# Performance work log

Hardware: AMD Instinct MI355X
Metric: run time of the kernel (lower is better)

Reference implementation:

```python
import jax, jax.numpy as jnp
import numpy as np

LEAKY_SLOPE = 0.01  # torch nn.LeakyReLU default

def leaky_relu(x):
    return jnp.where(x >= 0, x, LEAKY_SLOPE * x)

def setup_inputs() -> dict:
    key = jax.random.key(0)
    ks = jax.random.split(key, 11)
    B, F, C_IN, H, K, D = 2048, 512, 3, 64, 8, 128  # batch, features, expand, layer_conf[0], bucket_num, bucket_dim
    ASR, MM, OUT = 128, 768, 256
    proj_in = ASR + MM + F * D
    inp = {
        "stat_features": jax.random.uniform(ks[0], (B, F), dtype=jnp.float32),
        "asr_embeddings": jax.random.normal(ks[1], (B, ASR), dtype=jnp.float32),
        "mm_embeddings": jax.random.normal(ks[2], (B, MM), dtype=jnp.float32),
        "linear1_w": jax.random.normal(ks[3], (F, C_IN, H), dtype=jnp.float32) * (1.0 / np.sqrt(C_IN)),
        "linear1_b": jax.random.normal(ks[4], (F, 1, H), dtype=jnp.float32),
        "linear2_w": jax.random.normal(ks[5], (F, H, K), dtype=jnp.float32) * (1.0 / np.sqrt(H)),
        "linear2_b": jax.random.normal(ks[6], (F, 1, K), dtype=jnp.float32),
        "tau": jnp.ones((F, 1, K), dtype=jnp.float32),
        "emb": jax.random.normal(ks[7], (F, K, D), dtype=jnp.float32),
        "proj_w": jax.random.normal(ks[8], (OUT, proj_in), dtype=jnp.float32) * (1.0 / np.sqrt(proj_in)),
        "proj_b": jax.random.normal(ks[9], (OUT,), dtype=jnp.float32) * 0.01,
    }
    return inp

def reference(stat_features, asr_embeddings, mm_embeddings,
              linear1_w, linear1_b, linear2_w, linear2_b, tau, emb,
              proj_w, proj_b):
    # sanitize: NaN -> 0, negatives -> 0
    x = stat_features
    x = jnp.where(jnp.isnan(x) | (x < 0.0), 0.0, x)  # [B, F]

    # auto_dis: per-feature tiny MLP. x is expanded to 3 identical copies -> [B,F,1,3]
    # matmul with [F,3,H] == einsum over the 3 copies.
    B, F = x.shape
    x3 = jnp.broadcast_to(x[:, :, None], (B, F, 3))           # [B,F,3]
    h = jnp.einsum('bfc,fch->bfh', x3, linear1_w) + linear1_b[:, 0, :]  # [B,F,H]
    h = jnp.where(h >= 0, h, LEAKY_SLOPE * h)
    s = jnp.einsum('bfh,fhk->bfk', h, linear2_w) + linear2_b[:, 0, :]   # [B,F,K]
    s = jnp.where(s >= 0, s, LEAKY_SLOPE * s)
    s = s * tau[:, 0, :]
    p = jax.nn.softmax(s, axis=-1)                            # [B,F,K]
    y = jnp.einsum('bfk,fkd->bfd', p, emb)                    # [B,F,D]
    y = y.reshape(B, -1)                                      # [B, F*D] (fc = Identity)

    z = jnp.concatenate([asr_embeddings, mm_embeddings, y], axis=1)
    out = jax.nn.relu(z @ proj_w.T + proj_b)                  # [B, 256]
    return out
```

## Files before the change

kernel.cpp:

```cpp
#include <hip/hip_runtime.h>
#include <hip/hip_bf16.h>
#include <math.h>

#define LEAKY 0.01f
#define B_    2048
#define F_    512
#define H_    64
#define K_    8
#define D_    128
#define ASR_  128
#define MM_   768
#define OUT_  256
#define PROJ_IN 66432
#define ZK    4992
#define NSPLIT 8


typedef unsigned short u16;
typedef u16   u16x8 __attribute__((ext_vector_type(8)));
typedef short s16x8 __attribute__((ext_vector_type(8)));
typedef float f32x4 __attribute__((ext_vector_type(4)));

__device__ __forceinline__ u16 f2bf(float x) {
  unsigned int u = __float_as_uint(x);
  u += 0x7fffu + ((u >> 16) & 1u);
  return (u16)(u >> 16);
}

#define PRODUCER_BLOCKS (512 + 1024 + 896 + 224)
#define QS 40
#define FS 164

__global__ __launch_bounds__(256) void producer_kernel(
    const float* __restrict__ stat, const float* __restrict__ w1,
    const float* __restrict__ b1v, const float* __restrict__ w2,
    const float* __restrict__ b2v, const float* __restrict__ tauv,
    const float* __restrict__ pw, const float* __restrict__ emb,
    const float* __restrict__ asr, const float* __restrict__ mm,
    u16* __restrict__ A0, u16* __restrict__ Pf, u16* __restrict__ Wn) {
  __shared__ __align__(16) char smem[15616];
  const int bid = blockIdx.x;
  const int t = threadIdx.x;

  if (bid < 512) {
    const int f0 = (bid >> 3) * 8;
    const int o0 = (bid & 7) * 32;
    float* s_pw = (float*)smem;
    const int fl = t >> 5, k = (t >> 2) & 7, dq = t & 3;
    float4 e[8];
    {
      const float* ep = emb + ((size_t)(f0 + fl) * 8 + k) * 128 + dq * 32;
      #pragma unroll
      for (int j = 0; j < 8; ++j) e[j] = *(const float4*)(ep + j * 4);
    }
    const int cq = (t >> 3) & 3, ci = t & 7;
    const int wofs = (t >> 5) * FS + cq * QS + ci * 4;
    const float* pwbase = pw + 896 + (size_t)f0 * 128 + (size_t)o0 * PROJ_IN + t * 4;
#define LD(R) (*(const float4*)(pwbase + (size_t)(R) * PROJ_IN))
    float4 nx0 = LD(0), nx1 = LD(1), nx2 = LD(2);
    *(float4*)(s_pw + wofs) = nx0;
    nx0 = LD(3);
    asm volatile("s_waitcnt lgkmcnt(0)" ::: "memory");
    __builtin_amdgcn_s_barrier();
    u16* wdst = Wn + (size_t)o0 * ZK + 896 + (size_t)(f0 + fl) * 8 + k;
    for (int r = 0; r < 32; ++r) {
      float* buf  = s_pw + (r & 1) * (8 * FS);
      float* nbuf = s_pw + ((r + 1) & 1) * (8 * FS);
      if (r + 1 < 32) *(float4*)(nbuf + wofs) = nx1;
      nx1 = nx2; nx2 = nx0;
      if (r + 4 < 32) nx0 = LD(r + 4);
      const float* pp = buf + fl * FS + dq * QS;
      float gp0 = 0.f, gp1 = 0.f;
      #pragma unroll
      for (int j = 0; j < 8; ++j) {
        float4 p4 = *(const float4*)(pp + j * 4);
        gp0 = fmaf(e[j].x, p4.x, gp0);
        gp1 = fmaf(e[j].y, p4.y, gp1);
        gp0 = fmaf(e[j].z, p4.z, gp0);
        gp1 = fmaf(e[j].w, p4.w, gp1);
      }
      float g = gp0 + gp1;
      g += __shfl_xor(g, 1);
      g += __shfl_xor(g, 2);
      if (dq == 0) wdst[(size_t)r * ZK] = f2bf(g);
      asm volatile("s_waitcnt lgkmcnt(0)" ::: "memory");
      __builtin_amdgcn_s_barrier();
    }
#undef LD
  } else if (bid < 1536) {
    const int pb = bid - 512;
    const int f0 = (pb & 127) * 4;
    const int b0 = (pb >> 7) * 256;
    float* s_w1s = (float*)(smem);
    float* s_b1  = (float*)(smem + 1024);
    float* s_w2  = (float*)(smem + 2048);
    float* s_b2  = (float*)(smem + 10240);
    float* s_tau = (float*)(smem + 10368);
    float* s_x   = (float*)(smem + 10496);
    {
      int fl = t >> 6, h = t & 63;
      const float* wf = w1 + (size_t)(f0 + fl) * 192;
      s_w1s[fl * 64 + h] = wf[h] + wf[64 + h] + wf[128 + h];
      s_b1[fl * 64 + h] = b1v[(size_t)(f0 + fl) * 64 + h];
    }
    for (int i = t; i < 4 * 512; i += 256) {
      int fl = i >> 9, idx = i & 511;
      s_w2[fl * 512 + idx] = w2[(size_t)(f0 + fl) * 512 + idx];
    }
    if (t < 32) {
      s_b2[t]  = b2v[f0 * 8 + t];
      s_tau[t] = tauv[f0 * 8 + t];
    }
    {
      float4 sv = *(const float4*)(stat + (size_t)(b0 + t) * F_ + f0);
      float* xr = s_x + t * 5;
      xr[0] = (sv.x >= 0.f) ? sv.x : 0.f;
      xr[1] = (sv.y >= 0.f) ? sv.y : 0.f;
      xr[2] = (sv.z >= 0.f) ? sv.z : 0.f;
      xr[3] = (sv.w >= 0.f) ? sv.w : 0.f;
    }
    __syncthreads();

    const int w = t >> 6;
    const int lane = t & 63;
    const float* w1p = s_w1s + w * 64;
    const float* b1p = s_b1 + w * 64;
    const float* w2p = s_w2 + w * 512;
    float x[4];
    #pragma unroll
    for (int p = 0; p < 4; ++p) x[p] = s_x[(lane + 64 * p) * 5 + w];
    float acc[4][8] = {{0.f}};
    #pragma unroll 4
    for (int i = 0; i < 64; ++i) {
      float wv = w1p[i], bv = b1p[i];
      float4 wa = *(const float4*)(w2p + i * 8);
      float4 wb = *(const float4*)(w2p + i * 8 + 4);
      #pragma unroll
      for (int p = 0; p < 4; ++p) {
        float h0 = fmaf(x[p], wv, bv);
        float h = fmaf(LEAKY, fminf(h0, 0.f), fmaxf(h0, 0.f));
        acc[p][0] = fmaf(h, wa.x, acc[p][0]);
        acc[p][1] = fmaf(h, wa.y, acc[p][1]);
        acc[p][2] = fmaf(h, wa.z, acc[p][2]);
        acc[p][3] = fmaf(h, wa.w, acc[p][3]);
        acc[p][4] = fmaf(h, wb.x, acc[p][4]);
        acc[p][5] = fmaf(h, wb.y, acc[p][5]);
        acc[p][6] = fmaf(h, wb.z, acc[p][6]);
        acc[p][7] = fmaf(h, wb.w, acc[p][7]);
      }
    }
    #pragma unroll
    for (int p = 0; p < 4; ++p) {
      float s[K_];
      float m = -1e30f;
      #pragma unroll
      for (int kk = 0; kk < K_; ++kk) {
        float v = acc[p][kk] + s_b2[w * 8 + kk];
        v = (v >= 0.f) ? v : LEAKY * v;
        v *= s_tau[w * 8 + kk];
        s[kk] = v;
        m = fmaxf(m, v);
      }
      float sum = 0.f;
      #pragma unroll
      for (int kk = 0; kk < K_; ++kk) { s[kk] = __expf(s[kk] - m); sum += s[kk]; }
      float inv = 1.f / sum;
      u16x8 hv;
      #pragma unroll
      for (int kk = 0; kk < K_; ++kk) hv[kk] = f2bf(s[kk] * inv);
      *(u16x8*)(Pf + ((size_t)(f0 + w) * B_ + b0 + lane + 64 * p) * 8) = hv;
    }
  } else if (bid < 2432) {
    const int item = bid - 1536;
    const int cidx = item * 256 + t;
    const int r = cidx / 112, c = cidx % 112;
    float4 v0, v1;
    if (c < 16) {
      const float* s = asr + (size_t)r * ASR_ + c * 8;
      v0 = *(const float4*)(s); v1 = *(const float4*)(s + 4);
    } else {
      const float* s = mm + (size_t)r * MM_ + (c - 16) * 8;
      v0 = *(const float4*)(s); v1 = *(const float4*)(s + 4);
    }
    u16x8 hv = {f2bf(v0.x), f2bf(v0.y), f2bf(v0.z), f2bf(v0.w),
                f2bf(v1.x), f2bf(v1.y), f2bf(v1.z), f2bf(v1.w)};
    *(u16x8*)(A0 + (size_t)r * 896 + c * 8) = hv;
  } else {
    const int item = bid - 2432;
    #pragma unroll
    for (int rr = 0; rr < 4; ++rr) {
      int idx = item * 1024 + rr * 256 + t;
      int o = idx / 896, j = idx % 896;
      Wn[(size_t)o * ZK + j] = f2bf(pw[(size_t)o * PROJ_IN + j]);
    }
  }
}

#define SAS 72
__global__ __launch_bounds__(256) void gemm_kernel(
    const u16* __restrict__ A0, const u16* __restrict__ Pf,
    const u16* __restrict__ Wn, float* __restrict__ part) {
  const int bm0 = blockIdx.x * 64;
  const int bn0 = blockIdx.y * 64;
  const int kz  = blockIdx.z;
  const int it0 = kz * 10;
  const int itn = (kz == 7) ? 8 : 10;
  __shared__ u16 sA[64 * SAS];
  __shared__ u16 sB[64 * SAS];
  const int t = threadIdx.x;
  const int w = t >> 6, L = t & 63;
  const int l16 = L & 15, q8 = (L >> 4) * 8;
  const int wm = (w >> 1) * 32, wn = (w & 1) * 32;
  const int row = t >> 2, lk = t & 3;
  const int pp = t >> 5, pg = t & 31;
  f32x4 acc[2][2] = {{{0.f,0.f,0.f,0.f},{0.f,0.f,0.f,0.f}},
                     {{0.f,0.f,0.f,0.f},{0.f,0.f,0.f,0.f}}};
  u16x8 ra[2], rb[2];

#define LOAD_TILES(IT)                                                        \
  {                                                                           \
    const int k0_ = (IT) * 64;                                                \
    if (k0_ < 896) {                                                          \
      const u16* s_ = A0 + (size_t)(bm0 + row) * 896 + k0_ + lk * 8;          \
      ra[0] = *(const u16x8*)(s_);                                            \
      ra[1] = *(const u16x8*)(s_ + 32);                                       \
    } else {                                                                  \
      const int fb_ = (k0_ - 896) >> 3;                                       \
      const u16* s_ = Pf + ((size_t)(fb_ + pp) * B_ + bm0 + pg) * 8;          \
      ra[0] = *(const u16x8*)(s_);                                            \
      ra[1] = *(const u16x8*)(s_ + 256);                        \
    }                                                                         \
    const u16* sb_ = Wn + (size_t)(bn0 + row) * ZK + k0_ + lk * 8;            \
    rb[0] = *(const u16x8*)(sb_);                                             \
    rb[1] = *(const u16x8*)(sb_ + 32);                                        \
  }

#define STORE_TILES(IT)                                                       \
  {                                                                           \
    if ((IT) * 64 < 896) {                                                    \
      *(u16x8*)&sA[row * SAS + lk * 8]      = ra[0];                          \
      *(u16x8*)&sA[row * SAS + lk * 8 + 32] = ra[1];                          \
    } else {                                                                  \
      *(u16x8*)&sA[pg * SAS + pp * 8]        = ra[0];                         \
      *(u16x8*)&sA[(pg + 32) * SAS + pp * 8] = ra[1];                         \
    }                                                                         \
    *(u16x8*)&sB[row * SAS + lk * 8]      = rb[0];                            \
    *(u16x8*)&sB[row * SAS + lk * 8 + 32] = rb[1];                            \
  }

  LOAD_TILES(it0);
  for (int it = it0; it < it0 + itn; ++it) {
    __syncthreads();
    STORE_TILES(it);
    __syncthreads();
    if (it + 1 < it0 + itn) LOAD_TILES(it + 1);
    #pragma unroll
    for (int ks = 0; ks < 2; ++ks) {
      s16x8 a0 = *(const s16x8*)&sA[(wm + l16) * SAS + ks * 32 + q8];
      s16x8 a1 = *(const s16x8*)&sA[(wm + 16 + l16) * SAS + ks * 32 + q8];
      s16x8 b0 = *(const s16x8*)&sB[(wn + l16) * SAS + ks * 32 + q8];
      s16x8 b1 = *(const s16x8*)&sB[(wn + 16 + l16) * SAS + ks * 32 + q8];
      acc[0][0] = __builtin_amdgcn_mfma_f32_16x16x32_bf16(a0, b0, acc[0][0], 0, 0, 0);
      acc[0][1] = __builtin_amdgcn_mfma_f32_16x16x32_bf16(a0, b1, acc[0][1], 0, 0, 0);
      acc[1][0] = __builtin_amdgcn_mfma_f32_16x16x32_bf16(a1, b0, acc[1][0], 0, 0, 0);
      acc[1][1] = __builtin_amdgcn_mfma_f32_16x16x32_bf16(a1, b1, acc[1][1], 0, 0, 0);
    }
  }
#undef LOAD_TILES
#undef STORE_TILES

  float* dst = part + (size_t)kz * B_ * OUT_;
  #pragma unroll
  for (int mf = 0; mf < 2; ++mf) {
    const int r0 = bm0 + wm + mf * 16 + (L >> 4) * 4;
    #pragma unroll
    for (int nf = 0; nf < 2; ++nf) {
      const int col = bn0 + wn + nf * 16 + l16;
      #pragma unroll
      for (int i = 0; i < 4; ++i)
        dst[(size_t)(r0 + i) * OUT_ + col] = acc[mf][nf][i];
    }
  }
}

__global__ __launch_bounds__(256) void combine_kernel(
    const float* __restrict__ part, const float* __restrict__ pb,
    float* __restrict__ out) {
  const int idx4 = (blockIdx.x * 256 + threadIdx.x) * 4;
  const int o = idx4 & (OUT_ - 1);
  float4 bv = *(const float4*)(pb + o);
  float4 r = bv;
  #pragma unroll
  for (int kz = 0; kz < NSPLIT; ++kz) {
    float4 a = *(const float4*)(part + (size_t)kz * B_ * OUT_ + idx4);
    r.x += a.x; r.y += a.y; r.z += a.z; r.w += a.w;
  }
  r.x = r.x > 0.f ? r.x : 0.f;
  r.y = r.y > 0.f ? r.y : 0.f;
  r.z = r.z > 0.f ? r.z : 0.f;
  r.w = r.w > 0.f ? r.w : 0.f;
  *(float4*)(out + idx4) = r;
}

extern "C" void kernel_launch(void* const* d_in, const int* in_sizes, int n_in,
                              void* d_out, int out_size, void* d_ws, size_t ws_size,
                              hipStream_t stream) {
  (void)in_sizes; (void)n_in; (void)out_size; (void)ws_size;
  const float* stat = (const float*)d_in[0];
  const float* asr  = (const float*)d_in[1];
  const float* mm   = (const float*)d_in[2];
  const float* w1   = (const float*)d_in[3];
  const float* b1   = (const float*)d_in[4];
  const float* w2   = (const float*)d_in[5];
  const float* b2   = (const float*)d_in[6];
  const float* tau  = (const float*)d_in[7];
  const float* emb  = (const float*)d_in[8];
  const float* pw   = (const float*)d_in[9];
  const float* pb   = (const float*)d_in[10];
  float* out = (float*)d_out;
  char* ws = (char*)d_ws;
  u16*   A0   = (u16*)(ws);
  u16*   Pf   = (u16*)(ws + 3670016);
  u16*   Wn   = (u16*)(ws + 20447232);
  float* part = (float*)(ws + 23003136);

  producer_kernel<<<PRODUCER_BLOCKS, 256, 0, stream>>>(
      stat, w1, b1, w2, b2, tau, pw, emb, asr, mm, A0, Pf, Wn);
  gemm_kernel<<<dim3(B_ / 64, OUT_ / 64, NSPLIT), 256, 0, stream>>>(
      A0, Pf, Wn, part);
  combine_kernel<<<B_ * OUT_ / 1024, 256, 0, stream>>>(part, pb, out);
}
```

Baseline: 158.8 us.

## Read per-feature w2/b2/tau via uniform scalar loads; halve GEMM split-K count

The softmax-bucket producer stops staging linear2 weights, bias and tau in shared memory. Each wave instead reads them straight from global memory through a wave-uniform pointer made with readfirstlane, so the compiler can issue scalar loads. This drops LDS traffic and cuts the barrier-covered staging phase. Separately, the GEMM split-K factor goes from 8 to 4, giving fewer partial outputs to reduce but fewer blocks running in parallel.

```diff
diff --git a/kernel.cpp b/kernel.cpp
--- a/kernel.cpp
+++ b/kernel.cpp
@@ -13,7 +13,7 @@
 #define OUT_  256
 #define PROJ_IN 66432
 #define ZK    4992
-#define NSPLIT 8
+#define NSPLIT 4
 
 
 typedef unsigned short u16;
@@ -93,39 +93,31 @@
     const int b0 = (pb >> 7) * 256;
     float* s_w1s = (float*)(smem);
     float* s_b1  = (float*)(smem + 1024);
-    float* s_w2  = (float*)(smem + 2048);
-    float* s_b2  = (float*)(smem + 10240);
-    float* s_tau = (float*)(smem + 10368);
-    float* s_x   = (float*)(smem + 10496);
+    float* s_x   = (float*)(smem + 2048);
     {
       int fl = t >> 6, h = t & 63;
       const float* wf = w1 + (size_t)(f0 + fl) * 192;
       s_w1s[fl * 64 + h] = wf[h] + wf[64 + h] + wf[128 + h];
       s_b1[fl * 64 + h] = b1v[(size_t)(f0 + fl) * 64 + h];
     }
-    for (int i = t; i < 4 * 512; i += 256) {
-      int fl = i >> 9, idx = i & 511;
-      s_w2[fl * 512 + idx] = w2[(size_t)(f0 + fl) * 512 + idx];
-    }
-    if (t < 32) {
-      s_b2[t]  = b2v[f0 * 8 + t];
-      s_tau[t] = tauv[f0 * 8 + t];
-    }
     {
       float4 sv = *(const float4*)(stat + (size_t)(b0 + t) * F_ + f0);
-      float* xr = s_x + t * 5;
-      xr[0] = (sv.x >= 0.f) ? sv.x : 0.f;
-      xr[1] = (sv.y >= 0.f) ? sv.y : 0.f;
-      xr[2] = (sv.z >= 0.f) ? sv.z : 0.f;
-      xr[3] = (sv.w >= 0.f) ? sv.w : 0.f;
+      float* xr_ = s_x + t * 5;
+      xr_[0] = (sv.x >= 0.f) ? sv.x : 0.f;
+      xr_[1] = (sv.y >= 0.f) ? sv.y : 0.f;
+      xr_[2] = (sv.z >= 0.f) ? sv.z : 0.f;
+      xr_[3] = (sv.w >= 0.f) ? sv.w : 0.f;
     }
     __syncthreads();
 
     const int w = t >> 6;
+    const int wu = __builtin_amdgcn_readfirstlane(w);
     const int lane = t & 63;
     const float* w1p = s_w1s + w * 64;
     const float* b1p = s_b1 + w * 64;
-    const float* w2p = s_w2 + w * 512;
+    const float* w2u  = w2   + (size_t)(f0 + wu) * 512;
+    const float* b2u  = b2v  + (size_t)(f0 + wu) * 8;
+    const float* tauu = tauv + (size_t)(f0 + wu) * 8;
     float x[4];
     #pragma unroll
     for (int p = 0; p < 4; ++p) x[p] = s_x[(lane + 64 * p) * 5 + w];
@@ -133,8 +125,8 @@
     #pragma unroll 4
     for (int i = 0; i < 64; ++i) {
       float wv = w1p[i], bv = b1p[i];
-      float4 wa = *(const float4*)(w2p + i * 8);
-      float4 wb = *(const float4*)(w2p + i * 8 + 4);
+      float4 wa = *(const float4*)(w2u + i * 8);
+      float4 wb = *(const float4*)(w2u + i * 8 + 4);
       #pragma unroll
       for (int p = 0; p < 4; ++p) {
         float h0 = fmaf(x[p], wv, bv);
@@ -155,9 +147,9 @@
       float m = -1e30f;
       #pragma unroll
       for (int kk = 0; kk < K_; ++kk) {
-        float v = acc[p][kk] + s_b2[w * 8 + kk];
+        float v = acc[p][kk] + b2u[kk];
         v = (v >= 0.f) ? v : LEAKY * v;
-        v *= s_tau[w * 8 + kk];
+        v *= tauu[kk];
         s[kk] = v;
         m = fmaxf(m, v);
       }
@@ -203,8 +195,8 @@
   const int bm0 = blockIdx.x * 64;
   const int bn0 = blockIdx.y * 64;
   const int kz  = blockIdx.z;
-  const int it0 = kz * 10;
-  const int itn = (kz == 7) ? 8 : 10;
+  const int it0 = kz * 20;
+  const int itn = (kz == 3) ? 18 : 20;
   __shared__ u16 sA[64 * SAS];
   __shared__ u16 sB[64 * SAS];
   const int t = threadIdx.x;
```

New measurement: 157.4 us. Within noise of the previous version (-0.9%).
